# Kernel optimization log

Measured on AMD Instinct MI355X. Metric: run time of the kernel, lower is better.

Reference implementation:

```python
import jax, jax.numpy as jnp
import numpy as np

BN_EPS = 1e-5
L2_EPS = 1e-12  # F.normalize eps
K = 9           # kernel_size (dilation=1 so effective k = 9)
GROUPS = 4      # hard-coded groups in MRConv2d


def setup_inputs() -> dict:
    key = jax.random.key(0)
    k1, k2, k3 = jax.random.split(key, 3)
    B, C, H, W = 32, 192, 28, 28
    Cout = 384
    x = jax.random.normal(k1, (B, C, H, W), jnp.float32)
    # Conv2d(2C, Cout, 1, groups=4) weight is [Cout, 2C//4, 1, 1]; store as [Cout, 2C//4]
    fan_in = 2 * C // GROUPS
    conv_w = jax.random.normal(k2, (Cout, fan_in), jnp.float32) * np.sqrt(2.0 / fan_in)
    conv_b = jax.random.normal(k3, (Cout,), jnp.float32) * 0.05
    gamma = jnp.ones((Cout,), jnp.float32)
    beta = jnp.zeros((Cout,), jnp.float32)
    return {"x": x, "conv_w": conv_w, "conv_b": conv_b, "gamma": gamma, "beta": beta}


def _knn_idx(xf, k):
    """xf: (B, C, N) -> nn_idx: (B, N, k) via L2-normalized pairwise distance + topk."""
    xn = xf / jnp.maximum(jnp.linalg.norm(xf, axis=1, keepdims=True), L2_EPS)
    xt = xn.transpose(0, 2, 1)                       # (B, N, C)
    sq = jnp.sum(xt * xt, axis=-1, keepdims=True)    # (B, N, 1)
    inner = jnp.einsum('bnc,bmc->bnm', xt, xt)       # (B, N, N)
    dist = sq - 2.0 * inner + sq.transpose(0, 2, 1)
    _, nn_idx = jax.lax.top_k(-dist, k)              # (B, N, k)
    return nn_idx


def _forward(x, conv_w, conv_b, gamma, beta):
    B, C, H, W = x.shape
    N = H * W
    xf = x.reshape(B, C, N)
    # KNN graph built on detached features (torch: no_grad + x.detach for y when r=1)
    y = jax.lax.stop_gradient(xf)
    nn_idx = _knn_idx(y, K)                                            # (B, N, K)
    # gather neighbor features: xj[b,c,n,kk] = y[b,c,nn_idx[b,n,kk]]
    xj = jax.vmap(lambda yb, ib: yb[:, ib])(y, nn_idx)                 # (B, C, N, K)
    # max-relative: max_k (x_j - x_i); center gather of edge_index[1] is just xf
    rel = jnp.max(xj - xf[:, :, :, None], axis=-1)                     # (B, C, N)
    # cat([x.unsqueeze(2), rel.unsqueeze(2)], dim=2).reshape(B, 2C, N): channel-interleaved
    h = jnp.stack([xf, rel], axis=2).reshape(B, 2 * C, N)
    # grouped 1x1 conv, groups=4
    Cin = 2 * C
    Cout = conv_w.shape[0]
    hg = h.reshape(B, GROUPS, Cin // GROUPS, N)
    wg = conv_w.reshape(GROUPS, Cout // GROUPS, Cin // GROUPS)
    out = jnp.einsum('bgin,goi->bgon', hg, wg).reshape(B, Cout, N)
    out = out + conv_b[None, :, None]
    # BatchNorm2d (training-mode batch stats, biased variance)
    mean = jnp.mean(out, axis=(0, 2), keepdims=True)
    var = jnp.var(out, axis=(0, 2), keepdims=True)
    out = (out - mean) * jax.lax.rsqrt(var + BN_EPS)
    out = out * gamma[None, :, None] + beta[None, :, None]
    # exact (erf-based) GELU, matching torch.nn.GELU default
    out = jax.nn.gelu(out, approximate=False)
    return out.reshape(B, Cout, H, W)


def reference(x, conv_w, conv_b, gamma, beta):
    return _forward(x, conv_w, conv_b, gamma, beta)
```

## Files before the change

kernel.cpp:

```cpp
#include <hip/hip_runtime.h>

#define B_    32
#define C_    192
#define N_    784
#define NP_   1024
#define K_    9
#define COUT_ 384
#define NPTS_ (B_ * N_)
#define NTILES_ 224
#define DKW_  832

typedef __attribute__((ext_vector_type(8))) short short8;
typedef __attribute__((ext_vector_type(4))) float f32x4;

__device__ __forceinline__ unsigned int ford(float f) {
  unsigned int u = __float_as_uint(f);
  return u ^ ((u & 0x80000000u) ? 0xFFFFFFFFu : 0x80000000u);
}
__device__ __forceinline__ unsigned short f2bf(float f) {
  unsigned int u = __float_as_uint(f);
  u += 0x7FFFu + ((u >> 16) & 1u);
  return (unsigned short)(u >> 16);
}
__device__ __forceinline__ float bf2f(unsigned short h) {
  return __uint_as_float(((unsigned int)h) << 16);
}

__global__ __launch_bounds__(256) void norm_kernel(
    const float* __restrict__ x, short8* __restrict__ fragH,
    short8* __restrict__ fragL, float* __restrict__ sqp,
    float* __restrict__ xT) {
  int t = threadIdx.x;
  int pl = t & 63, cg = t >> 6;
  int p = blockIdx.x * 64 + pl;
  int b = p / N_, n = p % N_;
  const float* xb = x + (size_t)b * C_ * N_ + n;

  __shared__ float Tl[64][193];
  __shared__ float red[4][64];
  __shared__ float nrmS[64];

  float part = 0.f;
  #pragma unroll
  for (int j = 0; j < 48; j++) {
    float v = xb[(size_t)(cg * 48 + j) * N_];
    Tl[pl][cg * 48 + j] = v;
    part = __fmaf_rn(v, v, part);
  }
  red[cg][pl] = part;
  __syncthreads();
  if (t < 64) {
    float ssq = __fadd_rn(__fadd_rn(red[0][t], red[1][t]),
                          __fadd_rn(red[2][t], red[3][t]));
    nrmS[t] = fmaxf(__fsqrt_rn(ssq), 1e-12f);
  }
  __syncthreads();

  {
    size_t base = (size_t)blockIdx.x * 64 * C_;
    for (int idx = t; idx < 64 * C_; idx += 256)
      xT[base + idx] = Tl[idx / C_][idx % C_];
  }

  float nrm = nrmS[pl];
  int g = n >> 4, li = n & 15;
  float p2 = 0.f;
  #pragma unroll
  for (int s = 0; s < 6; s++) {
    int kslot = cg * 6 + s;
    int ks = kslot >> 2, kq = kslot & 3;
    union { short8 v; unsigned short u[8]; } ph, plo;
    #pragma unroll
    for (int j = 0; j < 8; j++) {
      float a = __fdiv_rn(Tl[pl][kslot * 8 + j], nrm);
      unsigned short h = f2bf(a);
      ph.u[j]  = h;
      plo.u[j] = f2bf(__fsub_rn(a, bf2f(h)));
      p2 = __fmaf_rn(a, a, p2);
    }
    size_t idx = (((size_t)b * 6 + ks) * 64 + g) * 64 + (kq * 16 + li);
    fragH[idx] = ph.v;
    fragL[idx] = plo.v;
  }
  red[cg][pl] = p2;
  __syncthreads();
  if (t < 64) {
    float sq = __fadd_rn(__fadd_rn(red[0][t], red[1][t]),
                         __fadd_rn(red[2][t], red[3][t]));
    int pp = blockIdx.x * 64 + t;
    sqp[(size_t)(pp / N_) * NP_ + (pp % N_)] = sq;
  }
}

__global__ __launch_bounds__(256, 3) void knn_kernel(
    const short8* __restrict__ fragH, const short8* __restrict__ fragL,
    const float* __restrict__ sqp, int* __restrict__ nn9) {
  int wg = blockIdx.x;
  int r = wg & 7, j = wg >> 3;
  int b  = r + 8 * (j / 49);
  int qt = j % 49;
  int q0 = qt * 16;
  int t = threadIdx.x, lane = t & 63, w = t >> 6;

  __shared__ unsigned int dkS[16][DKW_];

  for (int i = t; i < 16 * 48; i += 256)
    dkS[i / 48][784 + i % 48] = 0xFFFFFFFFu;
  __syncthreads();

  const float* sqb = sqp + (size_t)b * NP_;
  const short8* fH = fragH + (size_t)b * 6 * 64 * 64;
  const short8* fL = fragL + (size_t)b * 6 * 64 * 64;

  int colL = lane & 15, rq = lane >> 4;

  float qsv[4];
  #pragma unroll
  for (int rr = 0; rr < 4; rr++) qsv[rr] = sqb[q0 + rq * 4 + rr];

  short8 aH[6], aL[6];
  #pragma unroll
  for (int ks = 0; ks < 6; ks++) {
    aH[ks] = fH[((size_t)ks * 64 + qt) * 64 + lane];
    aL[ks] = fL[((size_t)ks * 64 + qt) * 64 + lane];
  }

  const int wstart = (w == 0) ? 0 : (w == 1) ? 13 : (w == 2) ? 26 : 39;
  const int wend   = (w == 0) ? 13 : (w == 1) ? 26 : (w == 2) ? 39 : 49;

  int g = wstart;
  for (; g + 1 < wend; g += 2) {
    int g0 = g, g1 = g + 1;
    short8 B0h[6], B0l[6], B1h[6], B1l[6];
    #pragma unroll
    for (int ks = 0; ks < 6; ks++) {
      B0h[ks] = fH[((size_t)ks * 64 + g0) * 64 + lane];
      B0l[ks] = fL[((size_t)ks * 64 + g0) * 64 + lane];
      B1h[ks] = fH[((size_t)ks * 64 + g1) * 64 + lane];
      B1l[ks] = fL[((size_t)ks * 64 + g1) * 64 + lane];
    }
    float cs0 = sqb[g0 * 16 + colL];
    float cs1 = sqb[g1 * 16 + colL];
    f32x4 a00 = {0.f, 0.f, 0.f, 0.f}, a01 = a00, a02 = a00;
    f32x4 a10 = a00, a11 = a00, a12 = a00;
    #pragma unroll
    for (int ks = 0; ks < 6; ks++) {
      a00 = __builtin_amdgcn_mfma_f32_16x16x32_bf16(aH[ks], B0h[ks], a00, 0, 0, 0);
      a01 = __builtin_amdgcn_mfma_f32_16x16x32_bf16(aH[ks], B0l[ks], a01, 0, 0, 0);
      a02 = __builtin_amdgcn_mfma_f32_16x16x32_bf16(aL[ks], B0h[ks], a02, 0, 0, 0);
      a10 = __builtin_amdgcn_mfma_f32_16x16x32_bf16(aH[ks], B1h[ks], a10, 0, 0, 0);
      a11 = __builtin_amdgcn_mfma_f32_16x16x32_bf16(aH[ks], B1l[ks], a11, 0, 0, 0);
      a12 = __builtin_amdgcn_mfma_f32_16x16x32_bf16(aL[ks], B1h[ks], a12, 0, 0, 0);
    }
    #pragma unroll
    for (int rr = 0; rr < 4; rr++) {
      int row = rq * 4 + rr;
      float qs = qsv[rr];
      float g0v = __fadd_rn(__fadd_rn(a00[rr], a01[rr]), a02[rr]);
      float g1v = __fadd_rn(__fadd_rn(a10[rr], a11[rr]), a12[rr]);
      float d0 = __fadd_rn(__fsub_rn(qs, __fmul_rn(2.0f, g0v)), cs0);
      float d1 = __fadd_rn(__fsub_rn(qs, __fmul_rn(2.0f, g1v)), cs1);
      dkS[row][g0 * 16 + colL] = ford(d0);
      dkS[row][g1 * 16 + colL] = ford(d1);
    }
  }
  if (g < wend) {
    int g0 = g;
    short8 B0h[6], B0l[6];
    #pragma unroll
    for (int ks = 0; ks < 6; ks++) {
      B0h[ks] = fH[((size_t)ks * 64 + g0) * 64 + lane];
      B0l[ks] = fL[((size_t)ks * 64 + g0) * 64 + lane];
    }
    float cs0 = sqb[g0 * 16 + colL];
    f32x4 a00 = {0.f, 0.f, 0.f, 0.f}, a01 = a00, a02 = a00;
    #pragma unroll
    for (int ks = 0; ks < 6; ks++) {
      a00 = __builtin_amdgcn_mfma_f32_16x16x32_bf16(aH[ks], B0h[ks], a00, 0, 0, 0);
      a01 = __builtin_amdgcn_mfma_f32_16x16x32_bf16(aH[ks], B0l[ks], a01, 0, 0, 0);
      a02 = __builtin_amdgcn_mfma_f32_16x16x32_bf16(aL[ks], B0h[ks], a02, 0, 0, 0);
    }
    #pragma unroll
    for (int rr = 0; rr < 4; rr++) {
      int row = rq * 4 + rr;
      float qs = qsv[rr];
      float g0v = __fadd_rn(__fadd_rn(a00[rr], a01[rr]), a02[rr]);
      float d0 = __fadd_rn(__fsub_rn(qs, __fmul_rn(2.0f, g0v)), cs0);
      dkS[row][g0 * 16 + colL] = ford(d0);
    }
  }
  __syncthreads();

  for (int s = 0; s < 4; s++) {
    int row = w * 4 + s;
    unsigned int bv = 0xFFFFFFFFu; int bi = lane;
    #pragma unroll
    for (int it = 0; it < 13; it++) {
      unsigned int k = dkS[row][lane + 64 * it];
      if (k < bv) { bv = k; bi = lane + 64 * it; }
    }
    int* o = nn9 + ((size_t)b * N_ + q0 + row) * K_;
    for (int kk = 0; kk < K_; kk++) {
      unsigned long long mk = ((unsigned long long)bv << 10) | (unsigned int)bi;
      #pragma unroll
      for (int off = 1; off < 64; off <<= 1) {
        unsigned long long v2 = __shfl_xor(mk, off);
        mk = v2 < mk ? v2 : mk;
      }
      int widx = (int)(mk & 1023u);
      if (lane == 0) o[kk] = widx;
      if ((widx & 63) == lane) {
        dkS[row][widx] = 0xFFFFFFFFu;
        bv = 0xFFFFFFFFu; bi = lane;
        #pragma unroll
        for (int it = 0; it < 13; it++) {
          unsigned int k = dkS[row][lane + 64 * it];
          if (k < bv) { bv = k; bi = lane + 64 * it; }
        }
      }
    }
  }
}

__global__ __launch_bounds__(256) void fconv_kernel(
    const float* __restrict__ xT, const int* __restrict__ nn9,
    const float* __restrict__ w, const float* __restrict__ bias,
    unsigned short* __restrict__ outpre, float* __restrict__ psum,
    float* __restrict__ pss) {
  int nt = blockIdx.x;
  int g  = blockIdx.y;
  int b  = blockIdx.z;
  int n0 = nt * 112;
  int t = threadIdx.x;

  __shared__ unsigned short Wl[96][98];
  __shared__ float Hl[96][112];
  __shared__ unsigned short Il[112][K_];

  const int* isrc = nn9 + ((size_t)b * N_ + n0) * K_;
  for (int i = t; i < 112 * K_; i += 256)
    Il[i / K_][i % K_] = (unsigned short)isrc[i];
  const float* wsrc = w + (size_t)(g * 96) * 96;
  for (int i = t; i < 96 * 96; i += 256)
    Wl[i / 96][i % 96] = f2bf(wsrc[i]);
  __syncthreads();

  if (t < 224) {
    int nl = t >> 1, half = t & 1;
    const float* xrow = xT + ((size_t)b * N_ + n0 + nl) * C_ + g * 48 + half * 24;
    float xv[24], mx[24];
    #pragma unroll
    for (int j = 0; j < 24; j += 4) {
      float4 v = *(const float4*)(xrow + j);
      xv[j] = v.x; xv[j + 1] = v.y; xv[j + 2] = v.z; xv[j + 3] = v.w;
      mx[j] = -1e30f; mx[j + 1] = -1e30f; mx[j + 2] = -1e30f; mx[j + 3] = -1e30f;
    }
    #pragma unroll
    for (int k = 0; k < K_; k++) {
      int idx = Il[nl][k];
      const float* nrow = xT + ((size_t)b * N_ + idx) * C_ + g * 48 + half * 24;
      #pragma unroll
      for (int j = 0; j < 24; j += 4) {
        float4 v = *(const float4*)(nrow + j);
        mx[j]     = fmaxf(mx[j], v.x);
        mx[j + 1] = fmaxf(mx[j + 1], v.y);
        mx[j + 2] = fmaxf(mx[j + 2], v.z);
        mx[j + 3] = fmaxf(mx[j + 3], v.w);
      }
    }
    #pragma unroll
    for (int j = 0; j < 24; j++) {
      int cl = half * 24 + j;
      Hl[2 * cl][nl]     = xv[j];
      Hl[2 * cl + 1][nl] = mx[j] - xv[j];
    }
  }
  __syncthreads();

  int tx = t & 15, ty = t >> 4;
  int tidx = b * 7 + nt;

  float o[6][7];
  #pragma unroll
  for (int i = 0; i < 6; i++)
    #pragma unroll
    for (int j = 0; j < 7; j++) o[i][j] = 0.f;

  for (int k = 0; k < 96; k++) {
    float wv[6];
    #pragma unroll
    for (int i = 0; i < 6; i++) wv[i] = bf2f(Wl[ty * 6 + i][k]);
    #pragma unroll
    for (int j = 0; j < 7; j++) {
      float hv = Hl[k][tx * 7 + j];
      #pragma unroll
      for (int i = 0; i < 6; i++) o[i][j] = __fmaf_rn(wv[i], hv, o[i][j]);
    }
  }

  #pragma unroll
  for (int i = 0; i < 6; i++) {
    int co = g * 96 + ty * 6 + i;
    float bv = bias[co];
    float s = 0.f, s2 = 0.f;
    unsigned short* orow =
        outpre + ((size_t)b * COUT_ + co) * N_ + n0 + tx * 7;
    #pragma unroll
    for (int j = 0; j < 7; j++) {
      float v = o[i][j] + bv;
      orow[j] = f2bf(v);
      s += v; s2 += v * v;
    }
    #pragma unroll
    for (int off = 1; off < 16; off <<= 1) {
      s  += __shfl_xor(s, off);
      s2 += __shfl_xor(s2, off);
    }
    if (tx == 0) {
      psum[co * NTILES_ + tidx] = s;
      pss [co * NTILES_ + tidx] = s2;
    }
  }
}

__global__ __launch_bounds__(64) void stats_kernel(
    const float* __restrict__ psum, const float* __restrict__ pss,
    const float* __restrict__ gamma, const float* __restrict__ beta,
    float* __restrict__ af, float* __restrict__ bf) {
  int co = blockIdx.x;
  int l = threadIdx.x;
  double s = 0.0, s2 = 0.0;
  for (int i = l; i < NTILES_; i += 64) {
    s  += (double)psum[co * NTILES_ + i];
    s2 += (double)pss [co * NTILES_ + i];
  }
  #pragma unroll
  for (int o = 32; o > 0; o >>= 1) { s += __shfl_xor(s, o); s2 += __shfl_xor(s2, o); }
  if (l == 0) {
    const double cnt = (double)NPTS_;
    double mean = s / cnt;
    double var  = s2 / cnt - mean * mean;
    double rstd = 1.0 / sqrt(var + 1e-5);
    double a = (double)gamma[co] * rstd;
    af[co] = (float)a;
    bf[co] = (float)((double)beta[co] - mean * a);
  }
}

__global__ __launch_bounds__(256) void act_kernel(
    const unsigned short* __restrict__ outpre, const float* __restrict__ af,
    const float* __restrict__ bf, float* __restrict__ out) {
  size_t i = ((size_t)blockIdx.x * 256 + threadIdx.x) * 8;
  int co = (int)((i / N_) % COUT_);
  float a = af[co], c = bf[co];
  union { uint4 u4; unsigned short us[8]; } pk;
  pk.u4 = *reinterpret_cast<const uint4*>(outpre + i);
  const float is2 = 0.70710678118654752f;
  float r[8];
  #pragma unroll
  for (int j = 0; j < 8; j++) {
    float y = __fmaf_rn(a, bf2f(pk.us[j]), c);
    r[j] = 0.5f * y * (1.0f + erff(y * is2));
  }
  float4 r0 = {r[0], r[1], r[2], r[3]};
  float4 r1 = {r[4], r[5], r[6], r[7]};
  *reinterpret_cast<float4*>(out + i) = r0;
  *reinterpret_cast<float4*>(out + i + 4) = r1;
}

extern "C" void kernel_launch(void* const* d_in, const int* in_sizes, int n_in,
                              void* d_out, int out_size, void* d_ws, size_t ws_size,
                              hipStream_t stream) {
  const float* x      = (const float*)d_in[0];
  const float* conv_w = (const float*)d_in[1];
  const float* conv_b = (const float*)d_in[2];
  const float* gamma  = (const float*)d_in[3];
  const float* beta   = (const float*)d_in[4];
  float* out = (float*)d_out;

  float* buf0 = (float*)d_ws;
  short8* fragH = (short8*)buf0;
  short8* fragL = (short8*)(buf0 + 3145728);
  unsigned short* outpre = (unsigned short*)buf0;
  float*  sqp   = buf0 + 9633792;
  int*    nn9   = (int*)(buf0 + 9666560);
  float*  xT    = buf0 + 9892352;
  float*  psum  = buf0 + 14709248;
  float*  pss   = psum + COUT_ * NTILES_;
  float*  af    = pss + COUT_ * NTILES_;
  float*  bfv   = af + COUT_;

  hipLaunchKernelGGL(norm_kernel, dim3(NPTS_ / 64), dim3(256), 0, stream,
                     x, fragH, fragL, sqp, xT);
  hipLaunchKernelGGL(knn_kernel, dim3(49 * B_), dim3(256), 0, stream,
                     fragH, fragL, sqp, nn9);
  hipLaunchKernelGGL(fconv_kernel, dim3(7, 4, B_), dim3(256), 0, stream,
                     xT, nn9, conv_w, conv_b, outpre, psum, pss);
  hipLaunchKernelGGL(stats_kernel, dim3(COUT_), dim3(64), 0, stream,
                     psum, pss, gamma, beta, af, bfv);
  hipLaunchKernelGGL(act_kernel, dim3((B_ * COUT_ * N_) / (256 * 8)), dim3(256), 0, stream,
                     outpre, af, bfv, out);
}
```

Before: 189.0 us.

## Keep KNN distances in registers with per-wave partial top-k and merge

Replaces the 16x832 shared-memory distance buffer in the KNN kernel with per-lane register arrays. Each wave computes a partial top-9 per query row via 16-lane shuffles over its own column slice, stores the candidates in a small shared array, and a final 36-candidate merge picks the global top-9. This cuts LDS usage so occupancy can rise (launch bounds 3 to 4) and removes the LDS rescans. The cost is more registers and redundant selection work in every wave.

```diff
diff --git a/kernel.cpp b/kernel.cpp
--- a/kernel.cpp
+++ b/kernel.cpp
@@ -8,7 +8,6 @@
 #define COUT_ 384
 #define NPTS_ (B_ * N_)
 #define NTILES_ 224
-#define DKW_  832
 
 typedef __attribute__((ext_vector_type(8))) short short8;
 typedef __attribute__((ext_vector_type(4))) float f32x4;
@@ -92,7 +91,7 @@
   }
 }
 
-__global__ __launch_bounds__(256, 3) void knn_kernel(
+__global__ __launch_bounds__(256, 4) void knn_kernel(
     const short8* __restrict__ fragH, const short8* __restrict__ fragL,
     const float* __restrict__ sqp, int* __restrict__ nn9) {
   int wg = blockIdx.x;
@@ -102,11 +101,7 @@
   int q0 = qt * 16;
   int t = threadIdx.x, lane = t & 63, w = t >> 6;
 
-  __shared__ unsigned int dkS[16][DKW_];
-
-  for (int i = t; i < 16 * 48; i += 256)
-    dkS[i / 48][784 + i % 48] = 0xFFFFFFFFu;
-  __syncthreads();
+  __shared__ unsigned long long partialS[4][16][K_];
 
   const float* sqb = sqp + (size_t)b * NP_;
   const short8* fH = fragH + (size_t)b * 6 * 64 * 64;
@@ -126,21 +121,29 @@
   }
 
   const int wstart = (w == 0) ? 0 : (w == 1) ? 13 : (w == 2) ? 26 : 39;
-  const int wend   = (w == 0) ? 13 : (w == 1) ? 26 : (w == 2) ? 39 : 49;
-
-  int g = wstart;
-  for (; g + 1 < wend; g += 2) {
-    int g0 = g, g1 = g + 1;
+  const int wend   = (w == 3) ? 49 : (wstart + 13);
+
+  unsigned int kreg[4][13];
+  #pragma unroll
+  for (int rr = 0; rr < 4; rr++)
+    #pragma unroll
+    for (int it = 0; it < 13; it++) kreg[rr][it] = 0xFFFFFFFFu;
+
+  #pragma unroll
+  for (int slot = 0; slot < 12; slot += 2) {
+    int g0 = wstart + slot, g1 = wstart + slot + 1;
+    bool v0 = g0 < wend, v1 = g1 < wend;
+    int g0c = v0 ? g0 : 48, g1c = v1 ? g1 : 48;
     short8 B0h[6], B0l[6], B1h[6], B1l[6];
     #pragma unroll
     for (int ks = 0; ks < 6; ks++) {
-      B0h[ks] = fH[((size_t)ks * 64 + g0) * 64 + lane];
-      B0l[ks] = fL[((size_t)ks * 64 + g0) * 64 + lane];
-      B1h[ks] = fH[((size_t)ks * 64 + g1) * 64 + lane];
-      B1l[ks] = fL[((size_t)ks * 64 + g1) * 64 + lane];
-    }
-    float cs0 = sqb[g0 * 16 + colL];
-    float cs1 = sqb[g1 * 16 + colL];
+      B0h[ks] = fH[((size_t)ks * 64 + g0c) * 64 + lane];
+      B0l[ks] = fL[((size_t)ks * 64 + g0c) * 64 + lane];
+      B1h[ks] = fH[((size_t)ks * 64 + g1c) * 64 + lane];
+      B1l[ks] = fL[((size_t)ks * 64 + g1c) * 64 + lane];
+    }
+    float cs0 = sqb[g0c * 16 + colL];
+    float cs1 = sqb[g1c * 16 + colL];
     f32x4 a00 = {0.f, 0.f, 0.f, 0.f}, a01 = a00, a02 = a00;
     f32x4 a10 = a00, a11 = a00, a12 = a00;
     #pragma unroll
@@ -154,25 +157,26 @@
     }
     #pragma unroll
     for (int rr = 0; rr < 4; rr++) {
-      int row = rq * 4 + rr;
       float qs = qsv[rr];
       float g0v = __fadd_rn(__fadd_rn(a00[rr], a01[rr]), a02[rr]);
       float g1v = __fadd_rn(__fadd_rn(a10[rr], a11[rr]), a12[rr]);
       float d0 = __fadd_rn(__fsub_rn(qs, __fmul_rn(2.0f, g0v)), cs0);
       float d1 = __fadd_rn(__fsub_rn(qs, __fmul_rn(2.0f, g1v)), cs1);
-      dkS[row][g0 * 16 + colL] = ford(d0);
-      dkS[row][g1 * 16 + colL] = ford(d1);
-    }
-  }
-  if (g < wend) {
-    int g0 = g;
+      if (v0) kreg[rr][slot]     = ford(d0);
+      if (v1) kreg[rr][slot + 1] = ford(d1);
+    }
+  }
+  {
+    int g0 = wstart + 12;
+    bool v0 = g0 < wend;
+    int g0c = v0 ? g0 : 48;
     short8 B0h[6], B0l[6];
     #pragma unroll
     for (int ks = 0; ks < 6; ks++) {
-      B0h[ks] = fH[((size_t)ks * 64 + g0) * 64 + lane];
-      B0l[ks] = fL[((size_t)ks * 64 + g0) * 64 + lane];
-    }
-    float cs0 = sqb[g0 * 16 + colL];
+      B0h[ks] = fH[((size_t)ks * 64 + g0c) * 64 + lane];
+      B0l[ks] = fL[((size_t)ks * 64 + g0c) * 64 + lane];
+    }
+    float cs0 = sqb[g0c * 16 + colL];
     f32x4 a00 = {0.f, 0.f, 0.f, 0.f}, a01 = a00, a02 = a00;
     #pragma unroll
     for (int ks = 0; ks < 6; ks++) {
@@ -182,42 +186,59 @@
     }
     #pragma unroll
     for (int rr = 0; rr < 4; rr++) {
-      int row = rq * 4 + rr;
       float qs = qsv[rr];
       float g0v = __fadd_rn(__fadd_rn(a00[rr], a01[rr]), a02[rr]);
       float d0 = __fadd_rn(__fsub_rn(qs, __fmul_rn(2.0f, g0v)), cs0);
-      dkS[row][g0 * 16 + colL] = ford(d0);
+      if (v0) kreg[rr][12] = ford(d0);
+    }
+  }
+
+  #pragma unroll
+  for (int rr = 0; rr < 4; rr++) {
+    int row = rq * 4 + rr;
+    unsigned int bv = 0xFFFFFFFFu; int bit = 0;
+    #pragma unroll
+    for (int it = 0; it < 13; it++)
+      if (kreg[rr][it] < bv) { bv = kreg[rr][it]; bit = it; }
+    for (int kk = 0; kk < K_; kk++) {
+      unsigned long long mk =
+          ((unsigned long long)bv << 10) |
+          (unsigned int)((wstart + bit) * 16 + colL);
+      #pragma unroll
+      for (int off = 1; off < 16; off <<= 1) {
+        unsigned long long v2 = __shfl_xor(mk, off);
+        mk = v2 < mk ? v2 : mk;
+      }
+      if (colL == 0) partialS[w][row][kk] = mk;
+      int col = (int)(mk & 1023u);
+      if ((col & 15) == colL) {
+        int slot = (col >> 4) - wstart;
+        #pragma unroll
+        for (int it = 0; it < 13; it++)
+          if (it == slot) kreg[rr][it] = 0xFFFFFFFFu;
+      }
+      bv = 0xFFFFFFFFu; bit = 0;
+      #pragma unroll
+      for (int it = 0; it < 13; it++)
+        if (kreg[rr][it] < bv) { bv = kreg[rr][it]; bit = it; }
     }
   }
   __syncthreads();
 
   for (int s = 0; s < 4; s++) {
     int row = w * 4 + s;
-    unsigned int bv = 0xFFFFFFFFu; int bi = lane;
-    #pragma unroll
-    for (int it = 0; it < 13; it++) {
-      unsigned int k = dkS[row][lane + 64 * it];
-      if (k < bv) { bv = k; bi = lane + 64 * it; }
-    }
+    unsigned long long v = (lane < 36)
+        ? partialS[lane / 9][row][lane % 9] : ~0ull;
     int* o = nn9 + ((size_t)b * N_ + q0 + row) * K_;
     for (int kk = 0; kk < K_; kk++) {
-      unsigned long long mk = ((unsigned long long)bv << 10) | (unsigned int)bi;
+      unsigned long long mk = v;
       #pragma unroll
       for (int off = 1; off < 64; off <<= 1) {
         unsigned long long v2 = __shfl_xor(mk, off);
         mk = v2 < mk ? v2 : mk;
       }
-      int widx = (int)(mk & 1023u);
-      if (lane == 0) o[kk] = widx;
-      if ((widx & 63) == lane) {
-        dkS[row][widx] = 0xFFFFFFFFu;
-        bv = 0xFFFFFFFFu; bi = lane;
-        #pragma unroll
-        for (int it = 0; it < 13; it++) {
-          unsigned int k = dkS[row][lane + 64 * it];
-          if (k < bv) { bv = k; bi = lane + 64 * it; }
-        }
-      }
+      if (lane == 0) o[kk] = (int)(mk & 1023u);
+      if (v == mk) v = ~0ull;
     }
   }
 }
```

Result: slower. 250.1 us (+32.3%).
